# Kernel optimization log

Hardware: AMD Instinct MI355X
Metric: run time of the kernel (lower is better)

Reference implementation:

```python
import jax, jax.numpy as jnp
import numpy as np

EPS = 1e-5

def _bn(x, g, b, m, v):
    # inference batchnorm: (x - mean) * rsqrt(var + eps) * gamma + beta
    return (x - m) * jax.lax.rsqrt(v + EPS) * g + b

def _relu6(x):
    return jnp.clip(x, 0.0, 6.0)

def setup_inputs() -> dict:
    key = jax.random.key(0)
    ks = jax.random.split(key, 20)
    N, Cin, Cout, K = 200000, 32, 32, 9  # K = 3^2 kernel offsets (dimension=2)
    H = int(round(Cin * 6))              # hidden = in_channels * expand_ratio = 192
    inp = {}
    inp["feats"] = jax.random.normal(ks[0], (N, Cin), jnp.float32)
    # rulebook neighbor map: -1 means no active neighbor at that kernel offset
    inp["neighbor_idx"] = jax.random.randint(ks[1], (N, K), -1, N, dtype=jnp.int32)
    # ME convs have bias=False by default
    inp["W1"] = jax.random.normal(ks[2], (Cin, H), jnp.float32) * 0.05
    inp["W2"] = jax.random.normal(ks[3], (K, H), jnp.float32) * 0.05   # channelwise (depthwise) kernel
    inp["W3"] = jax.random.normal(ks[4], (H, Cout), jnp.float32) * 0.05
    for i, (name, c) in enumerate([("1", H), ("2", H), ("3", Cout)]):
        base = 5 + 4 * i
        inp["g" + name] = 1.0 + 0.1 * jax.random.normal(ks[base], (c,), jnp.float32)
        inp["b" + name] = 0.1 * jax.random.normal(ks[base + 1], (c,), jnp.float32)
        inp["m" + name] = 0.1 * jax.random.normal(ks[base + 2], (c,), jnp.float32)
        inp["v" + name] = jax.random.uniform(ks[base + 3], (c,), jnp.float32, 0.5, 1.5)
    return inp

def _depthwise_sparse_conv(x, neighbor_idx, W2):
    # x: [N, H], neighbor_idx: [N, K] (-1 = missing), W2: [K, H]
    K = W2.shape[0]
    acc = jnp.zeros_like(x)
    safe = jnp.maximum(neighbor_idx, 0)
    valid = (neighbor_idx >= 0)
    for k in range(K):  # small fixed kernel loop; each gather streams [N, H]
        g = jnp.where(valid[:, k:k + 1], x[safe[:, k]], 0.0)
        acc = acc + g * W2[k]
    return acc

def reference(feats, neighbor_idx, W1, W2, W3,
              g1, b1, m1, v1, g2, b2, m2, v2, g3, b3, m3, v3):
    identity = feats
    x = _relu6(_bn(feats @ W1, g1, b1, m1, v1))          # 1x1 expand conv
    x = _depthwise_sparse_conv(x, neighbor_idx, W2)       # 3x3 depthwise sparse conv
    x = _relu6(_bn(x, g2, b2, m2, v2))
    x = _bn(x @ W3, g3, b3, m3, v3)                       # 1x1 project conv
    return x + identity                                   # residual (in==out, stride==1)
```

## Files before the change

kernel.cpp:

```cpp
#include <hip/hip_runtime.h>

#define EPS 1e-5f

typedef __bf16 bf16x8 __attribute__((ext_vector_type(8)));
typedef float f32x4 __attribute__((ext_vector_type(4)));

union BF8 { bf16x8 v; unsigned short u[8]; uint4 q; };

__device__ inline unsigned short f32_to_bf16(float f) {
    unsigned u = __builtin_bit_cast(unsigned, f);
    return (unsigned short)((u + 0x7FFFu + ((u >> 16) & 1u)) >> 16);
}
__device__ inline float relu6f(float x) { return fminf(fmaxf(x, 0.f), 6.f); }

__global__ __launch_bounds__(256) void k0_prep(
    const float* __restrict__ W1, const float* __restrict__ W3,
    const float* __restrict__ g1, const float* __restrict__ b1,
    const float* __restrict__ m1, const float* __restrict__ v1,
    const float* __restrict__ g2, const float* __restrict__ b2,
    const float* __restrict__ m2, const float* __restrict__ v2,
    const float* __restrict__ g3, const float* __restrict__ b3,
    const float* __restrict__ m3, const float* __restrict__ v3,
    unsigned short* __restrict__ w1t, unsigned short* __restrict__ w3t,
    float* __restrict__ bnc)
{
    const int gtid = blockIdx.x * 256 + threadIdx.x;
    const int gstr = gridDim.x * 256;
    for (int i = gtid; i < 6144; i += gstr) {
        int n = i >> 5, k = i & 31;
        w1t[i] = f32_to_bf16(W1[k * 192 + n]);
    }
    for (int i = gtid; i < 6144; i += gstr) {
        int n = i / 192, k = i - n * 192;
        w3t[i] = f32_to_bf16(W3[k * 32 + n]);
    }
    if (blockIdx.x == 0) {
        int t = threadIdx.x;
        const float Q = 255.f / 6.f;
        if (t < 192) {
            float s = g1[t] * rsqrtf(v1[t] + EPS);
            bnc[t] = s * Q; bnc[192 + t] = (b1[t] - m1[t] * s) * Q;
            float u = g2[t] * rsqrtf(v2[t] + EPS);
            bnc[384 + t] = u; bnc[576 + t] = b2[t] - m2[t] * u;
            if (t < 32) {
                float w = g3[t] * rsqrtf(v3[t] + EPS);
                bnc[768 + t] = w; bnc[800 + t] = b3[t] - m3[t] * w;
            }
        }
    }
}

__global__ __launch_bounds__(256) void k1_expand(
    const float* __restrict__ feats, const unsigned short* __restrict__ w1t,
    const float* __restrict__ bnc, unsigned char* __restrict__ x1, int N)
{
    __shared__ __align__(16) unsigned char outB[128 * 224];
    const int tid = threadIdx.x;
    const int rowbase = blockIdx.x * 128;
    const int lane = tid & 63, wave = tid >> 6;
    const int m = lane & 15, q = lane >> 4;

    bf16x8 bf[12];
#pragma unroll
    for (int t = 0; t < 12; ++t)
        bf[t] = *(const bf16x8*)(w1t + (16 * t + m) * 32 + q * 8);

#pragma unroll
    for (int p = 0; p < 2; ++p) {
        const int tile = wave * 2 + p;
        const int row = rowbase + tile * 16 + m;
        float4 f0 = {0.f,0.f,0.f,0.f}, f1 = {0.f,0.f,0.f,0.f};
        if (row < N) {
            f0 = *(const float4*)(feats + (size_t)row * 32 + q * 8);
            f1 = *(const float4*)(feats + (size_t)row * 32 + q * 8 + 4);
        }
        BF8 af;
        af.u[0] = f32_to_bf16(f0.x); af.u[1] = f32_to_bf16(f0.y);
        af.u[2] = f32_to_bf16(f0.z); af.u[3] = f32_to_bf16(f0.w);
        af.u[4] = f32_to_bf16(f1.x); af.u[5] = f32_to_bf16(f1.y);
        af.u[6] = f32_to_bf16(f1.z); af.u[7] = f32_to_bf16(f1.w);

        f32x4 acc[12];
#pragma unroll
        for (int t = 0; t < 12; ++t) {
            f32x4 z = {0.f, 0.f, 0.f, 0.f};
            acc[t] = __builtin_amdgcn_mfma_f32_16x16x32_bf16(af.v, bf[t], z, 0, 0, 0);
        }

#pragma unroll
        for (int t = 0; t < 12; ++t) {
            int c = 16 * t + m;
            float s = bnc[c], bb = bnc[192 + c];
#pragma unroll
            for (int i = 0; i < 4; ++i) {
                int r = tile * 16 + q * 4 + i;
                float y = fmaf(acc[t][i], s, bb);
                y = fminf(fmaxf(y, 0.f), 255.f);
                outB[r * 224 + c] = (unsigned char)(y + 0.5f);
            }
        }
    }
    __syncthreads();

#pragma unroll
    for (int j = 0; j < 6; ++j) {
        int i = j * 256 + tid;
        int r = i / 12, c = i % 12;
        int gr = rowbase + r;
        if (gr < N)
            *(uint4*)(x1 + (size_t)gr * 192 + c * 16) = *(const uint4*)(&outB[r * 224 + c * 16]);
    }
}

__global__ __launch_bounds__(192) void k2_fused(
    const unsigned char* __restrict__ x1, const int* __restrict__ nbr,
    const float* __restrict__ W2, const unsigned short* __restrict__ w3t,
    const float* __restrict__ bnc, const float* __restrict__ feats,
    float* __restrict__ out, int N)
{
    __shared__ __align__(16) unsigned short x2L[48 * 200];
    __shared__ __align__(16) int offL[48 * 12];
    const int tid = threadIdx.x;
    const int rowbase = blockIdx.x * 48;

    for (int i = tid; i < 432; i += 192) {
        int r = i / 9, k = i - r * 9;
        int n = rowbase + r;
        int idx = (n < N) ? nbr[(size_t)n * 9 + k] : -1;
        offL[r * 12 + k] = (idx < 0) ? -1 : idx * 192;
    }

    const int cg = tid % 48;
    const int slot = tid / 48;
    const int c0 = cg * 4;
    const char* x1b = (const char*)x1 + c0;

    const float DQ = 6.f / 255.f;
    float w2v[9][4];
#pragma unroll
    for (int k = 0; k < 9; ++k) {
        float4 w = *(const float4*)(W2 + k * 192 + c0);
        w2v[k][0] = w.x * DQ; w2v[k][1] = w.y * DQ; w2v[k][2] = w.z * DQ; w2v[k][3] = w.w * DQ;
    }
    float4 s2 = *(const float4*)(bnc + 384 + c0);
    float4 bb2 = *(const float4*)(bnc + 576 + c0);
    __syncthreads();

#pragma unroll
    for (int it = 0; it < 6; ++it) {
        int r0 = it * 8 + slot, r1 = r0 + 4;
        const int* nA = &offL[r0 * 12];
        const int* nB = &offL[r1 * 12];
        int4 a03 = *(const int4*)nA; int4 a47 = *(const int4*)(nA + 4); int a8 = nA[8];
        int4 b03 = *(const int4*)nB; int4 b47 = *(const int4*)(nB + 4); int b8 = nB[8];
        int offA[9] = {a03.x, a03.y, a03.z, a03.w, a47.x, a47.y, a47.z, a47.w, a8};
        int offB[9] = {b03.x, b03.y, b03.z, b03.w, b47.x, b47.y, b47.z, b47.w, b8};
        unsigned gA[9], gB[9];
#pragma unroll
        for (int k = 0; k < 9; ++k) {
            gA[k] = *(const unsigned*)(x1b + (offA[k] < 0 ? 0 : offA[k]));
            gB[k] = *(const unsigned*)(x1b + (offB[k] < 0 ? 0 : offB[k]));
        }
        float a0 = 0.f, a1 = 0.f, a2 = 0.f, a3 = 0.f;
        float c0f = 0.f, c1 = 0.f, c2 = 0.f, c3 = 0.f;
#pragma unroll
        for (int k = 0; k < 9; ++k) {
            unsigned ga = offA[k] >= 0 ? gA[k] : 0u;
            unsigned gb = offB[k] >= 0 ? gB[k] : 0u;
            a0 = fmaf((float)(ga & 0xFF),         w2v[k][0], a0);
            a1 = fmaf((float)((ga >> 8) & 0xFF),  w2v[k][1], a1);
            a2 = fmaf((float)((ga >> 16) & 0xFF), w2v[k][2], a2);
            a3 = fmaf((float)(ga >> 24),          w2v[k][3], a3);
            c0f = fmaf((float)(gb & 0xFF),         w2v[k][0], c0f);
            c1  = fmaf((float)((gb >> 8) & 0xFF),  w2v[k][1], c1);
            c2  = fmaf((float)((gb >> 16) & 0xFF), w2v[k][2], c2);
            c3  = fmaf((float)(gb >> 24),          w2v[k][3], c3);
        }
        a0 = relu6f(fmaf(a0, s2.x, bb2.x));
        a1 = relu6f(fmaf(a1, s2.y, bb2.y));
        a2 = relu6f(fmaf(a2, s2.z, bb2.z));
        a3 = relu6f(fmaf(a3, s2.w, bb2.w));
        c0f = relu6f(fmaf(c0f, s2.x, bb2.x));
        c1  = relu6f(fmaf(c1,  s2.y, bb2.y));
        c2  = relu6f(fmaf(c2,  s2.z, bb2.z));
        c3  = relu6f(fmaf(c3,  s2.w, bb2.w));
        uint2 pA, pB;
        pA.x = (unsigned)f32_to_bf16(a0) | ((unsigned)f32_to_bf16(a1) << 16);
        pA.y = (unsigned)f32_to_bf16(a2) | ((unsigned)f32_to_bf16(a3) << 16);
        pB.x = (unsigned)f32_to_bf16(c0f) | ((unsigned)f32_to_bf16(c1) << 16);
        pB.y = (unsigned)f32_to_bf16(c2)  | ((unsigned)f32_to_bf16(c3) << 16);
        *(uint2*)(&x2L[r0 * 200 + c0]) = pA;
        *(uint2*)(&x2L[r1 * 200 + c0]) = pB;
    }
    __syncthreads();

    const int lane = tid & 63;
    const int wave = tid >> 6;
    const int m = lane & 15;
    const int q = lane >> 4;

    bf16x8 bfrag[12];
#pragma unroll
    for (int s = 0; s < 6; ++s)
#pragma unroll
        for (int t = 0; t < 2; ++t)
            bfrag[s * 2 + t] = *(const bf16x8*)(w3t + (16 * t + m) * 192 + 32 * s + q * 8);

    f32x4 acc0 = {0.f, 0.f, 0.f, 0.f}, acc1 = {0.f, 0.f, 0.f, 0.f};
    const int rw = wave * 16;
#pragma unroll
    for (int s = 0; s < 6; ++s) {
        bf16x8 a = *reinterpret_cast<const bf16x8*>(&x2L[(rw + m) * 200 + 32 * s + q * 8]);
        acc0 = __builtin_amdgcn_mfma_f32_16x16x32_bf16(a, bfrag[s * 2 + 0], acc0, 0, 0, 0);
        acc1 = __builtin_amdgcn_mfma_f32_16x16x32_bf16(a, bfrag[s * 2 + 1], acc1, 0, 0, 0);
    }

#pragma unroll
    for (int t = 0; t < 2; ++t) {
        f32x4 acc = (t == 0) ? acc0 : acc1;
        int c = 16 * t + m;
        float s3 = bnc[768 + c], bb3 = bnc[800 + c];
#pragma unroll
        for (int i = 0; i < 4; ++i) {
            int r = rowbase + rw + q * 4 + i;
            if (r < N) {
                int o = r * 32 + c;
                out[o] = fmaf(acc[i], s3, bb3) + feats[o];
            }
        }
    }
}

extern "C" void kernel_launch(void* const* d_in, const int* in_sizes, int n_in,
                              void* d_out, int out_size, void* d_ws, size_t ws_size,
                              hipStream_t stream) {
    const float* feats = (const float*)d_in[0];
    const int*   nbr   = (const int*)d_in[1];
    const float* W1    = (const float*)d_in[2];
    const float* W2    = (const float*)d_in[3];
    const float* W3    = (const float*)d_in[4];
    const float* g1 = (const float*)d_in[5];
    const float* b1 = (const float*)d_in[6];
    const float* m1 = (const float*)d_in[7];
    const float* v1 = (const float*)d_in[8];
    const float* g2 = (const float*)d_in[9];
    const float* b2 = (const float*)d_in[10];
    const float* m2 = (const float*)d_in[11];
    const float* v2 = (const float*)d_in[12];
    const float* g3 = (const float*)d_in[13];
    const float* b3 = (const float*)d_in[14];
    const float* m3 = (const float*)d_in[15];
    const float* v3 = (const float*)d_in[16];
    float* out = (float*)d_out;

    const int N = in_sizes[0] / 32;

    char* ws = (char*)d_ws;
    unsigned char*  x1  = (unsigned char*)ws;
    unsigned short* w1t = (unsigned short*)(ws + (size_t)N * 192);
    unsigned short* w3t = w1t + 6144;
    float*          bnc = (float*)(w3t + 6144);

    k0_prep<<<dim3(32), dim3(256), 0, stream>>>(
        W1, W3, g1, b1, m1, v1, g2, b2, m2, v2, g3, b3, m3, v3, w1t, w3t, bnc);
    k1_expand<<<dim3((N + 127) / 128), dim3(256), 0, stream>>>(
        feats, w1t, bnc, x1, N);
    k2_fused<<<dim3((N + 47) / 48), dim3(192), 0, stream>>>(
        x1, nbr, W2, w3t, bnc, feats, out, N);
}
```

Baseline: 197.0 us.

## Merge prep, expand and gather stages into one persistent cooperative kernel

Replaces the three-kernel pipeline (weight prep, expand, fused gather+project) with a single persistent cooperative kernel. Each block computes its transposed bf16 weights and BN constants in registers, runs the expand phase over grid-strided 48-row tiles, does a grid-wide sync, then runs the depthwise gather and project phase. This removes two launch gaps and the prep kernel. In exchange every block redoes the weight conversion with strided global reads, the expand tile is smaller and issues more syncthreads, and the grid barrier plus the launch_bounds occupancy cap may limit latency hiding in the gather phase. A two-kernel fallback is kept for when cooperative launch fails.

```diff
diff --git a/kernel.cpp b/kernel.cpp
--- a/kernel.cpp
+++ b/kernel.cpp
@@ -1,4 +1,7 @@
 #include <hip/hip_runtime.h>
+#include <hip/hip_cooperative_groups.h>
+
+namespace cg = cooperative_groups;
 
 #define EPS 1e-5f
 
@@ -13,115 +16,135 @@
 }
 __device__ inline float relu6f(float x) { return fminf(fmaxf(x, 0.f), 6.f); }
 
-__global__ __launch_bounds__(256) void k0_prep(
-    const float* __restrict__ W1, const float* __restrict__ W3,
-    const float* __restrict__ g1, const float* __restrict__ b1,
-    const float* __restrict__ m1, const float* __restrict__ v1,
+struct P1 { bf16x8 bf[12]; float s[12], b[12]; };
+
+__device__ __forceinline__ void p1_init(P1& st,
+    const float* __restrict__ W1, const float* __restrict__ g1,
+    const float* __restrict__ b1, const float* __restrict__ m1,
+    const float* __restrict__ v1, int m, int q)
+{
+    const float Q = 255.f / 6.f;
+#pragma unroll
+    for (int t = 0; t < 12; ++t) {
+        int c = 16 * t + m;
+        BF8 tmp;
+#pragma unroll
+        for (int j = 0; j < 8; ++j)
+            tmp.u[j] = f32_to_bf16(W1[(q * 8 + j) * 192 + c]);
+        st.bf[t] = tmp.v;
+        float s = g1[c] * rsqrtf(v1[c] + EPS);
+        st.s[t] = s * Q;
+        st.b[t] = (b1[c] - m1[c] * s) * Q;
+    }
+}
+
+__device__ __forceinline__ void p1_tile(const P1& st, int tile, int N,
+    const float* __restrict__ feats, unsigned char* __restrict__ x1,
+    unsigned char* outB, int tid)
+{
+    const int lane = tid & 63, wave = tid >> 6;
+    const int m = lane & 15, q = lane >> 4;
+    const int rowbase = tile * 48;
+    const int row = rowbase + wave * 16 + m;
+
+    float4 f0 = {0.f,0.f,0.f,0.f}, f1v = {0.f,0.f,0.f,0.f};
+    if (row < N) {
+        f0  = *(const float4*)(feats + (size_t)row * 32 + q * 8);
+        f1v = *(const float4*)(feats + (size_t)row * 32 + q * 8 + 4);
+    }
+    BF8 af;
+    af.u[0] = f32_to_bf16(f0.x);  af.u[1] = f32_to_bf16(f0.y);
+    af.u[2] = f32_to_bf16(f0.z);  af.u[3] = f32_to_bf16(f0.w);
+    af.u[4] = f32_to_bf16(f1v.x); af.u[5] = f32_to_bf16(f1v.y);
+    af.u[6] = f32_to_bf16(f1v.z); af.u[7] = f32_to_bf16(f1v.w);
+
+#pragma unroll
+    for (int t = 0; t < 12; ++t) {
+        f32x4 z = {0.f, 0.f, 0.f, 0.f};
+        f32x4 acc = __builtin_amdgcn_mfma_f32_16x16x32_bf16(af.v, st.bf[t], z, 0, 0, 0);
+        int c = 16 * t + m;
+#pragma unroll
+        for (int i = 0; i < 4; ++i) {
+            float y = fmaf(acc[i], st.s[t], st.b[t]);
+            y = fminf(fmaxf(y, 0.f), 255.f);
+            outB[(wave * 16 + q * 4 + i) * 224 + c] = (unsigned char)(y + 0.5f);
+        }
+    }
+    __syncthreads();
+#pragma unroll
+    for (int j = 0; j < 3; ++j) {
+        int i = j * 64 + lane;
+        int r = i / 12, c = i % 12;
+        int grow = rowbase + wave * 16 + r;
+        if (grow < N)
+            *(uint4*)(x1 + (size_t)grow * 192 + c * 16) =
+                *(const uint4*)(&outB[(wave * 16 + r) * 224 + c * 16]);
+    }
+    __syncthreads();
+}
+
+struct P2 {
+    float w2v[9][4];
+    float s2[4], bb2[4];
+    bf16x8 bfrag[12];
+    float s3c[2], bb3c[2];
+};
+
+__device__ __forceinline__ void p2_init(P2& st,
+    const float* __restrict__ W2, const float* __restrict__ W3,
     const float* __restrict__ g2, const float* __restrict__ b2,
     const float* __restrict__ m2, const float* __restrict__ v2,
     const float* __restrict__ g3, const float* __restrict__ b3,
     const float* __restrict__ m3, const float* __restrict__ v3,
-    unsigned short* __restrict__ w1t, unsigned short* __restrict__ w3t,
-    float* __restrict__ bnc)
-{
-    const int gtid = blockIdx.x * 256 + threadIdx.x;
-    const int gstr = gridDim.x * 256;
-    for (int i = gtid; i < 6144; i += gstr) {
-        int n = i >> 5, k = i & 31;
-        w1t[i] = f32_to_bf16(W1[k * 192 + n]);
-    }
-    for (int i = gtid; i < 6144; i += gstr) {
-        int n = i / 192, k = i - n * 192;
-        w3t[i] = f32_to_bf16(W3[k * 32 + n]);
-    }
-    if (blockIdx.x == 0) {
-        int t = threadIdx.x;
-        const float Q = 255.f / 6.f;
-        if (t < 192) {
-            float s = g1[t] * rsqrtf(v1[t] + EPS);
-            bnc[t] = s * Q; bnc[192 + t] = (b1[t] - m1[t] * s) * Q;
-            float u = g2[t] * rsqrtf(v2[t] + EPS);
-            bnc[384 + t] = u; bnc[576 + t] = b2[t] - m2[t] * u;
-            if (t < 32) {
-                float w = g3[t] * rsqrtf(v3[t] + EPS);
-                bnc[768 + t] = w; bnc[800 + t] = b3[t] - m3[t] * w;
-            }
-        }
-    }
-}
-
-__global__ __launch_bounds__(256) void k1_expand(
-    const float* __restrict__ feats, const unsigned short* __restrict__ w1t,
-    const float* __restrict__ bnc, unsigned char* __restrict__ x1, int N)
-{
-    __shared__ __align__(16) unsigned char outB[128 * 224];
-    const int tid = threadIdx.x;
-    const int rowbase = blockIdx.x * 128;
+    int tid)
+{
+    const int cgi = tid % 48;
+    const int c0 = cgi * 4;
+    const int lane = tid & 63;
+    const int m = lane & 15, q = lane >> 4;
+    const float DQ = 6.f / 255.f;
+#pragma unroll
+    for (int k = 0; k < 9; ++k) {
+        float4 w = *(const float4*)(W2 + k * 192 + c0);
+        st.w2v[k][0] = w.x * DQ; st.w2v[k][1] = w.y * DQ;
+        st.w2v[k][2] = w.z * DQ; st.w2v[k][3] = w.w * DQ;
+    }
+#pragma unroll
+    for (int j = 0; j < 4; ++j) {
+        int c = c0 + j;
+        float u = g2[c] * rsqrtf(v2[c] + EPS);
+        st.s2[j] = u; st.bb2[j] = b2[c] - m2[c] * u;
+    }
+#pragma unroll
+    for (int s = 0; s < 6; ++s)
+#pragma unroll
+        for (int t = 0; t < 2; ++t) {
+            BF8 tmp;
+#pragma unroll
+            for (int j = 0; j < 8; ++j)
+                tmp.u[j] = f32_to_bf16(W3[(32 * s + q * 8 + j) * 32 + 16 * t + m]);
+            st.bfrag[s * 2 + t] = tmp.v;
+        }
+#pragma unroll
+    for (int t = 0; t < 2; ++t) {
+        int c = 16 * t + m;
+        float w = g3[c] * rsqrtf(v3[c] + EPS);
+        st.s3c[t] = w; st.bb3c[t] = b3[c] - m3[c] * w;
+    }
+}
+
+__device__ __forceinline__ void p2_tile(const P2& st, int tile, int N,
+    const unsigned char* __restrict__ x1, const int* __restrict__ nbr,
+    const float* __restrict__ feats, float* __restrict__ out,
+    unsigned short* x2L, int* offL, int tid)
+{
+    const int rowbase = tile * 48;
+    const int cgi = tid % 48;
+    const int slot = tid / 48;
+    const int c0 = cgi * 4;
+    const char* x1b = (const char*)x1 + c0;
     const int lane = tid & 63, wave = tid >> 6;
     const int m = lane & 15, q = lane >> 4;
-
-    bf16x8 bf[12];
-#pragma unroll
-    for (int t = 0; t < 12; ++t)
-        bf[t] = *(const bf16x8*)(w1t + (16 * t + m) * 32 + q * 8);
-
-#pragma unroll
-    for (int p = 0; p < 2; ++p) {
-        const int tile = wave * 2 + p;
-        const int row = rowbase + tile * 16 + m;
-        float4 f0 = {0.f,0.f,0.f,0.f}, f1 = {0.f,0.f,0.f,0.f};
-        if (row < N) {
-            f0 = *(const float4*)(feats + (size_t)row * 32 + q * 8);
-            f1 = *(const float4*)(feats + (size_t)row * 32 + q * 8 + 4);
-        }
-        BF8 af;
-        af.u[0] = f32_to_bf16(f0.x); af.u[1] = f32_to_bf16(f0.y);
-        af.u[2] = f32_to_bf16(f0.z); af.u[3] = f32_to_bf16(f0.w);
-        af.u[4] = f32_to_bf16(f1.x); af.u[5] = f32_to_bf16(f1.y);
-        af.u[6] = f32_to_bf16(f1.z); af.u[7] = f32_to_bf16(f1.w);
-
-        f32x4 acc[12];
-#pragma unroll
-        for (int t = 0; t < 12; ++t) {
-            f32x4 z = {0.f, 0.f, 0.f, 0.f};
-            acc[t] = __builtin_amdgcn_mfma_f32_16x16x32_bf16(af.v, bf[t], z, 0, 0, 0);
-        }
-
-#pragma unroll
-        for (int t = 0; t < 12; ++t) {
-            int c = 16 * t + m;
-            float s = bnc[c], bb = bnc[192 + c];
-#pragma unroll
-            for (int i = 0; i < 4; ++i) {
-                int r = tile * 16 + q * 4 + i;
-                float y = fmaf(acc[t][i], s, bb);
-                y = fminf(fmaxf(y, 0.f), 255.f);
-                outB[r * 224 + c] = (unsigned char)(y + 0.5f);
-            }
-        }
-    }
-    __syncthreads();
-
-#pragma unroll
-    for (int j = 0; j < 6; ++j) {
-        int i = j * 256 + tid;
-        int r = i / 12, c = i % 12;
-        int gr = rowbase + r;
-        if (gr < N)
-            *(uint4*)(x1 + (size_t)gr * 192 + c * 16) = *(const uint4*)(&outB[r * 224 + c * 16]);
-    }
-}
-
-__global__ __launch_bounds__(192) void k2_fused(
-    const unsigned char* __restrict__ x1, const int* __restrict__ nbr,
-    const float* __restrict__ W2, const unsigned short* __restrict__ w3t,
-    const float* __restrict__ bnc, const float* __restrict__ feats,
-    float* __restrict__ out, int N)
-{
-    __shared__ __align__(16) unsigned short x2L[48 * 200];
-    __shared__ __align__(16) int offL[48 * 12];
-    const int tid = threadIdx.x;
-    const int rowbase = blockIdx.x * 48;
 
     for (int i = tid; i < 432; i += 192) {
         int r = i / 9, k = i - r * 9;
@@ -129,21 +152,6 @@
         int idx = (n < N) ? nbr[(size_t)n * 9 + k] : -1;
         offL[r * 12 + k] = (idx < 0) ? -1 : idx * 192;
     }
-
-    const int cg = tid % 48;
-    const int slot = tid / 48;
-    const int c0 = cg * 4;
-    const char* x1b = (const char*)x1 + c0;
-
-    const float DQ = 6.f / 255.f;
-    float w2v[9][4];
-#pragma unroll
-    for (int k = 0; k < 9; ++k) {
-        float4 w = *(const float4*)(W2 + k * 192 + c0);
-        w2v[k][0] = w.x * DQ; w2v[k][1] = w.y * DQ; w2v[k][2] = w.z * DQ; w2v[k][3] = w.w * DQ;
-    }
-    float4 s2 = *(const float4*)(bnc + 384 + c0);
-    float4 bb2 = *(const float4*)(bnc + 576 + c0);
     __syncthreads();
 
 #pragma unroll
@@ -167,23 +175,23 @@
         for (int k = 0; k < 9; ++k) {
             unsigned ga = offA[k] >= 0 ? gA[k] : 0u;
             unsigned gb = offB[k] >= 0 ? gB[k] : 0u;
-            a0 = fmaf((float)(ga & 0xFF),         w2v[k][0], a0);
-            a1 = fmaf((float)((ga >> 8) & 0xFF),  w2v[k][1], a1);
-            a2 = fmaf((float)((ga >> 16) & 0xFF), w2v[k][2], a2);
-            a3 = fmaf((float)(ga >> 24),          w2v[k][3], a3);
-            c0f = fmaf((float)(gb & 0xFF),         w2v[k][0], c0f);
-            c1  = fmaf((float)((gb >> 8) & 0xFF),  w2v[k][1], c1);
-            c2  = fmaf((float)((gb >> 16) & 0xFF), w2v[k][2], c2);
-            c3  = fmaf((float)(gb >> 24),          w2v[k][3], c3);
-        }
-        a0 = relu6f(fmaf(a0, s2.x, bb2.x));
-        a1 = relu6f(fmaf(a1, s2.y, bb2.y));
-        a2 = relu6f(fmaf(a2, s2.z, bb2.z));
-        a3 = relu6f(fmaf(a3, s2.w, bb2.w));
-        c0f = relu6f(fmaf(c0f, s2.x, bb2.x));
-        c1  = relu6f(fmaf(c1,  s2.y, bb2.y));
-        c2  = relu6f(fmaf(c2,  s2.z, bb2.z));
-        c3  = relu6f(fmaf(c3,  s2.w, bb2.w));
+            a0 = fmaf((float)(ga & 0xFF),         st.w2v[k][0], a0);
+            a1 = fmaf((float)((ga >> 8) & 0xFF),  st.w2v[k][1], a1);
+            a2 = fmaf((float)((ga >> 16) & 0xFF), st.w2v[k][2], a2);
+            a3 = fmaf((float)(ga >> 24),          st.w2v[k][3], a3);
+            c0f = fmaf((float)(gb & 0xFF),         st.w2v[k][0], c0f);
+            c1  = fmaf((float)((gb >> 8) & 0xFF),  st.w2v[k][1], c1);
+            c2  = fmaf((float)((gb >> 16) & 0xFF), st.w2v[k][2], c2);
+            c3  = fmaf((float)(gb >> 24),          st.w2v[k][3], c3);
+        }
+        a0 = relu6f(fmaf(a0, st.s2[0], st.bb2[0]));
+        a1 = relu6f(fmaf(a1, st.s2[1], st.bb2[1]));
+        a2 = relu6f(fmaf(a2, st.s2[2], st.bb2[2]));
+        a3 = relu6f(fmaf(a3, st.s2[3], st.bb2[3]));
+        c0f = relu6f(fmaf(c0f, st.s2[0], st.bb2[0]));
+        c1  = relu6f(fmaf(c1,  st.s2[1], st.bb2[1]));
+        c2  = relu6f(fmaf(c2,  st.s2[2], st.bb2[2]));
+        c3  = relu6f(fmaf(c3,  st.s2[3], st.bb2[3]));
         uint2 pA, pB;
         pA.x = (unsigned)f32_to_bf16(a0) | ((unsigned)f32_to_bf16(a1) << 16);
         pA.y = (unsigned)f32_to_bf16(a2) | ((unsigned)f32_to_bf16(a3) << 16);
@@ -194,41 +202,97 @@
     }
     __syncthreads();
 
-    const int lane = tid & 63;
-    const int wave = tid >> 6;
-    const int m = lane & 15;
-    const int q = lane >> 4;
-
-    bf16x8 bfrag[12];
-#pragma unroll
-    for (int s = 0; s < 6; ++s)
-#pragma unroll
-        for (int t = 0; t < 2; ++t)
-            bfrag[s * 2 + t] = *(const bf16x8*)(w3t + (16 * t + m) * 192 + 32 * s + q * 8);
-
     f32x4 acc0 = {0.f, 0.f, 0.f, 0.f}, acc1 = {0.f, 0.f, 0.f, 0.f};
     const int rw = wave * 16;
 #pragma unroll
     for (int s = 0; s < 6; ++s) {
         bf16x8 a = *reinterpret_cast<const bf16x8*>(&x2L[(rw + m) * 200 + 32 * s + q * 8]);
-        acc0 = __builtin_amdgcn_mfma_f32_16x16x32_bf16(a, bfrag[s * 2 + 0], acc0, 0, 0, 0);
-        acc1 = __builtin_amdgcn_mfma_f32_16x16x32_bf16(a, bfrag[s * 2 + 1], acc1, 0, 0, 0);
+        acc0 = __builtin_amdgcn_mfma_f32_16x16x32_bf16(a, st.bfrag[s * 2 + 0], acc0, 0, 0, 0);
+        acc1 = __builtin_amdgcn_mfma_f32_16x16x32_bf16(a, st.bfrag[s * 2 + 1], acc1, 0, 0, 0);
     }
 
 #pragma unroll
     for (int t = 0; t < 2; ++t) {
         f32x4 acc = (t == 0) ? acc0 : acc1;
         int c = 16 * t + m;
-        float s3 = bnc[768 + c], bb3 = bnc[800 + c];
 #pragma unroll
         for (int i = 0; i < 4; ++i) {
             int r = rowbase + rw + q * 4 + i;
             if (r < N) {
                 int o = r * 32 + c;
-                out[o] = fmaf(acc[i], s3, bb3) + feats[o];
+                out[o] = fmaf(acc[i], st.s3c[t], st.bb3c[t]) + feats[o];
             }
         }
     }
+}
+
+__global__ __launch_bounds__(192, 3) void fused_coop(
+    const float* __restrict__ feats, const int* __restrict__ nbr,
+    const float* __restrict__ W1, const float* __restrict__ W2,
+    const float* __restrict__ W3,
+    const float* __restrict__ g1, const float* __restrict__ b1,
+    const float* __restrict__ m1, const float* __restrict__ v1,
+    const float* __restrict__ g2, const float* __restrict__ b2,
+    const float* __restrict__ m2, const float* __restrict__ v2,
+    const float* __restrict__ g3, const float* __restrict__ b3,
+    const float* __restrict__ m3, const float* __restrict__ v3,
+    unsigned char* __restrict__ x1, float* __restrict__ out,
+    int N, int nTiles)
+{
+    __shared__ __align__(16) unsigned char smem[21504];
+    const int tid = threadIdx.x;
+    const int lane = tid & 63;
+    const int m = lane & 15, q = lane >> 4;
+
+    {
+        P1 p1;
+        p1_init(p1, W1, g1, b1, m1, v1, m, q);
+        for (int tile = blockIdx.x; tile < nTiles; tile += gridDim.x)
+            p1_tile(p1, tile, N, feats, x1, smem, tid);
+    }
+
+    cg::this_grid().sync();
+
+    {
+        P2 p2;
+        p2_init(p2, W2, W3, g2, b2, m2, v2, g3, b3, m3, v3, tid);
+        unsigned short* x2L = (unsigned short*)smem;
+        int* offL = (int*)(smem + 19200);
+        for (int tile = blockIdx.x; tile < nTiles; tile += gridDim.x)
+            p2_tile(p2, tile, N, x1, nbr, feats, out, x2L, offL, tid);
+    }
+}
+
+__global__ __launch_bounds__(192) void k1f(
+    const float* __restrict__ feats,
+    const float* __restrict__ W1,
+    const float* __restrict__ g1, const float* __restrict__ b1,
+    const float* __restrict__ m1, const float* __restrict__ v1,
+    unsigned char* __restrict__ x1, int N)
+{
+    __shared__ __align__(16) unsigned char outB[48 * 224];
+    const int tid = threadIdx.x;
+    const int lane = tid & 63;
+    P1 p1;
+    p1_init(p1, W1, g1, b1, m1, v1, lane & 15, lane >> 4);
+    p1_tile(p1, blockIdx.x, N, feats, x1, outB, tid);
+}
+
+__global__ __launch_bounds__(192) void k2f(
+    const unsigned char* __restrict__ x1, const int* __restrict__ nbr,
+    const float* __restrict__ W2, const float* __restrict__ W3,
+    const float* __restrict__ g2, const float* __restrict__ b2,
+    const float* __restrict__ m2, const float* __restrict__ v2,
+    const float* __restrict__ g3, const float* __restrict__ b3,
+    const float* __restrict__ m3, const float* __restrict__ v3,
+    const float* __restrict__ feats, float* __restrict__ out, int N)
+{
+    __shared__ __align__(16) unsigned short x2L[48 * 200];
+    __shared__ __align__(16) int offL[48 * 12];
+    const int tid = threadIdx.x;
+    P2 p2;
+    p2_init(p2, W2, W3, g2, b2, m2, v2, g3, b3, m3, v3, tid);
+    p2_tile(p2, blockIdx.x, N, x1, nbr, feats, out, x2L, offL, tid);
 }
 
 extern "C" void kernel_launch(void* const* d_in, const int* in_sizes, int n_in,
@@ -253,18 +317,39 @@
     const float* v3 = (const float*)d_in[16];
     float* out = (float*)d_out;
 
-    const int N = in_sizes[0] / 32;
-
-    char* ws = (char*)d_ws;
-    unsigned char*  x1  = (unsigned char*)ws;
-    unsigned short* w1t = (unsigned short*)(ws + (size_t)N * 192);
-    unsigned short* w3t = w1t + 6144;
-    float*          bnc = (float*)(w3t + 6144);
-
-    k0_prep<<<dim3(32), dim3(256), 0, stream>>>(
-        W1, W3, g1, b1, m1, v1, g2, b2, m2, v2, g3, b3, m3, v3, w1t, w3t, bnc);
-    k1_expand<<<dim3((N + 127) / 128), dim3(256), 0, stream>>>(
-        feats, w1t, bnc, x1, N);
-    k2_fused<<<dim3((N + 47) / 48), dim3(192), 0, stream>>>(
-        x1, nbr, W2, w3t, bnc, feats, out, N);
-}
+    int N = in_sizes[0] / 32;
+    int nTiles = (N + 47) / 48;
+    unsigned char* x1 = (unsigned char*)d_ws;
+
+    int occ = 0;
+    hipError_t eo = hipOccupancyMaxActiveBlocksPerMultiprocessor(
+        &occ, (const void*)fused_coop, 192, 0);
+    int dev = 0, nCU = 0;
+    hipGetDevice(&dev);
+    hipDeviceGetAttribute(&nCU, hipDeviceAttributeMultiprocessorCount, dev);
+    if (nCU <= 0) nCU = 256;
+
+    bool coop_done = false;
+    if (eo == hipSuccess && occ > 0) {
+        int grid = occ * nCU;
+        if (grid > nTiles) grid = nTiles;
+        if (grid < 1) grid = 1;
+        void* args[] = {
+            (void*)&feats, (void*)&nbr, (void*)&W1, (void*)&W2, (void*)&W3,
+            (void*)&g1, (void*)&b1, (void*)&m1, (void*)&v1,
+            (void*)&g2, (void*)&b2, (void*)&m2, (void*)&v2,
+            (void*)&g3, (void*)&b3, (void*)&m3, (void*)&v3,
+            (void*)&x1, (void*)&out, (void*)&N, (void*)&nTiles
+        };
+        hipError_t el = hipLaunchCooperativeKernel(
+            (const void*)fused_coop, dim3(grid), dim3(192), args, 0, stream);
+        coop_done = (el == hipSuccess);
+    }
+
+    if (!coop_done) {
+        k1f<<<dim3(nTiles), dim3(192), 0, stream>>>(
+            feats, W1, g1, b1, m1, v1, x1, N);
+        k2f<<<dim3(nTiles), dim3(192), 0, stream>>>(
+            x1, nbr, W2, W3, g2, b2, m2, v2, g3, b3, m3, v3, feats, out, N);
+    }
+}
```

Measured after the change: 335.4 us. +70.3%, slower.
